# Optimization experiments

Hardware: AMD Instinct MI355X
Metric: run time of the kernel (lower is better)

The kernel has to match this reference:

```python
import jax, jax.numpy as jnp
import numpy as np
import math

N = 4264          # all_node_num
B = 256           # batch size
VIS = 784 + 50    # input_node_num + label_node_num
NG = 8            # number of color groups (Pegasus chromatic number is small)
GS = N // NG      # 533 nodes per group
SAMPLE_NUM = 10   # Gibbs sweeps (default 1000 in source; reduced for reference)
AVG_DEG = 15.0    # Pegasus graph degree ~15


def setup_inputs() -> dict:
    key = jax.random.key(0)
    k1, k2, k3, k4 = jax.random.split(key, 4)
    # spin state in {-1, +1}, shape [B, N]
    m = jnp.where(jax.random.normal(k1, (B, N)) >= 0, 1.0, -1.0).astype(jnp.float32)
    # sparse symmetric coupling matrix J: ~AVG_DEG neighbors per node, values randn*0.01
    upper_mask = jnp.triu(jax.random.uniform(k2, (N, N)) < (AVG_DEG / N), k=1)
    Jup = jax.random.normal(k3, (N, N), dtype=jnp.float32) * 0.01 * upper_mask
    J = Jup + Jup.T
    # bias H: log-odds constant on visible nodes, zero on hidden
    h_vis = math.log((VIS / N) / (1.0 - VIS / N))
    H = jnp.zeros((N,), dtype=jnp.float32).at[:VIS].set(h_vis)
    # color groups: disjoint partition of node indices, [NG, GS]
    groups = jax.random.permutation(k4, N).reshape(NG, GS).astype(jnp.int32)
    return {"m": m, "J": J, "H": H, "groups": groups, "sample_num": SAMPLE_NUM}


def reference(m, J, H, groups, sample_num):
    n_groups = groups.shape[0]

    def sweep(m, key):
        keys = jax.random.split(key, n_groups)
        for g in range(n_groups):          # small fixed set of color groups
            idx = groups[g]                # [GS]
            # I = sparse.mm(J[idx], m.T).T + H[idx]  ->  [B, GS]
            I = jnp.einsum('bn,gn->bg', m, J[idx]) + H[idx]
            r = jax.random.uniform(keys[g], I.shape, dtype=I.dtype) * 2.0 - 1.0
            m = m.at[:, idx].set(jnp.sign(jnp.tanh(I) - r))
        return m, None

    iter_keys = jax.random.split(jax.random.key(42), sample_num)
    m, _ = jax.lax.scan(sweep, m, iter_keys)
    return m
```

## Files before the change

kernel.cpp:

```cpp
#include <hip/hip_runtime.h>
#include <hip/hip_bf16.h>
#include <stdint.h>

#define NN 4264
#define BB 256
#define GSZ 533
#define NGRP 8
#define NSWEEP 10
#define NSTEP (NSWEEP * NGRP)
#define DMAX 48
#define DFIX 24
#define NF4 1066

struct Keys { unsigned k0[NSTEP]; unsigned k1[NSTEP]; };

#define TF_ROUND(x0, x1, r) { x0 += x1; x1 = (x1 << (r)) | (x1 >> (32 - (r))); x1 ^= x0; }
#define TF_BODY(K0, K1, C0, C1, O0, O1) {                                   \
  unsigned ks0 = (K0), ks1 = (K1), ks2 = (K0) ^ (K1) ^ 0x1BD11BDAu;          \
  unsigned x0 = (C0) + ks0, x1 = (C1) + ks1;                                 \
  TF_ROUND(x0, x1, 13) TF_ROUND(x0, x1, 15) TF_ROUND(x0, x1, 26) TF_ROUND(x0, x1, 6)  \
  x0 += ks1; x1 += ks2 + 1u;                                                 \
  TF_ROUND(x0, x1, 17) TF_ROUND(x0, x1, 29) TF_ROUND(x0, x1, 16) TF_ROUND(x0, x1, 24) \
  x0 += ks2; x1 += ks0 + 2u;                                                 \
  TF_ROUND(x0, x1, 13) TF_ROUND(x0, x1, 15) TF_ROUND(x0, x1, 26) TF_ROUND(x0, x1, 6)  \
  x0 += ks0; x1 += ks1 + 3u;                                                 \
  TF_ROUND(x0, x1, 17) TF_ROUND(x0, x1, 29) TF_ROUND(x0, x1, 16) TF_ROUND(x0, x1, 24) \
  x0 += ks1; x1 += ks2 + 4u;                                                 \
  TF_ROUND(x0, x1, 13) TF_ROUND(x0, x1, 15) TF_ROUND(x0, x1, 26) TF_ROUND(x0, x1, 6)  \
  x0 += ks2; x1 += ks0 + 5u;                                                 \
  (O0) = x0; (O1) = x1; }

static void tf_host(unsigned k0, unsigned k1, unsigned c0, unsigned c1,
                    unsigned* o0, unsigned* o1) {
  unsigned a, b;
  TF_BODY(k0, k1, c0, c1, a, b);
  *o0 = a; *o1 = b;
}

__device__ __forceinline__ void tf_dev(unsigned k0, unsigned k1, unsigned c0, unsigned c1,
                                       unsigned& o0, unsigned& o1) {
  TF_BODY(k0, k1, c0, c1, o0, o1);
}

__global__ __launch_bounds__(256) void build_ell(const float* __restrict__ J,
                                                 const int* __restrict__ groups,
                                                 unsigned* __restrict__ pack4,
                                                 int2* __restrict__ exact8,
                                                 int* __restrict__ deg,
                                                 float* __restrict__ marg) {
  const int wv = threadIdx.x >> 6, lane = threadIdx.x & 63;
  const int p = blockIdx.x * 4 + wv;
  if (p >= NN) return;
  const int node = groups[p];
  const float4* row = (const float4*)(J + (size_t)node * NN);
  int cnt = 0;
  float asum = 0.0f;
  for (int it = 0; it < (NF4 + 63) / 64; ++it) {
    const int q = it * 64 + lane;
    float4 v;
    if (q < NF4) v = row[q];
    else         v = make_float4(0.0f, 0.0f, 0.0f, 0.0f);
    const int c0 = q * 4;
#define COMP(X, CIDX) {                                                        \
      const bool nz = ((X) != 0.0f);                                           \
      const unsigned long long mk = __ballot(nz);                              \
      const int rk = cnt + __popcll(mk & ((1ull << lane) - 1ull));             \
      if (nz) {                                                                \
        if (rk < DFIX) {                                                       \
          const unsigned bits = __float_as_uint(X);                            \
          const unsigned bf = (bits + 0x7fffu + ((bits >> 16) & 1u)) >> 16;    \
          pack4[(size_t)p * DFIX + rk] = (bf << 16) | ((unsigned)(CIDX) << 2); \
          asum += fabsf(X);                                                    \
        }                                                                      \
        if (rk < DMAX)                                                         \
          exact8[(size_t)p * DMAX + rk] = make_int2((CIDX), __float_as_int(X));\
      }                                                                        \
      cnt += __popcll(mk); }
    COMP(v.x, c0 + 0) COMP(v.y, c0 + 1) COMP(v.z, c0 + 2) COMP(v.w, c0 + 3)
#undef COMP
  }
  for (int k = cnt + lane; k < DFIX; k += 64) pack4[(size_t)p * DFIX + k] = 0u;
  for (int s = 1; s < 64; s <<= 1) asum += __shfl_xor(asum, s, 64);
  if (lane == 0) {
    deg[p] = (cnt > DMAX) ? DMAX : cnt;
    marg[p] = asum * 0.001953125f + 2e-5f;
  }
}

__global__ __launch_bounds__(576) void gibbs(const float* __restrict__ m0,
                                             const float* __restrict__ H,
                                             const int* __restrict__ groups,
                                             const unsigned* __restrict__ pack4,
                                             const int2* __restrict__ exact8,
                                             const int* __restrict__ deg,
                                             const float* __restrict__ marg,
                                             float* __restrict__ out,
                                             Keys keys) {
  __shared__ float m_lds[NN];
  const int b = blockIdx.x;
  const int i = threadIdx.x;
  const bool active = (i < GSZ);

  for (int n = i; n < NN; n += 576) m_lds[n] = m0[(size_t)b * NN + n];

  int nodeg[NGRP];
  float hg[NGRP], mgg[NGRP];
  int dgg[NGRP];
  if (active) {
#pragma unroll
    for (int g = 0; g < NGRP; ++g) {
      const int p = g * GSZ + i;
      nodeg[g] = groups[p];
      hg[g] = H[nodeg[g]];
      dgg[g] = deg[p];
      mgg[g] = marg[p];
    }
  }
  __syncthreads();

  const unsigned c = (unsigned)(b * GSZ + i);

#pragma unroll 1
  for (int t = 0; t < NSWEEP; ++t) {
#pragma unroll
    for (int g = 0; g < NGRP; ++g) {
      const int step = t * NGRP + g;
      const unsigned k0 = keys.k0[step];
      const unsigned k1 = keys.k1[step];
      float nv = 0.0f;
      if (active) {
        const int p = g * GSZ + i;
        const uint4* q = (const uint4*)(pack4 + (size_t)p * DFIX);
        uint4 w0 = q[0], w1 = q[1], w2 = q[2], w3 = q[3], w4 = q[4], w5 = q[5];
        float a0 = 0.0f, a1 = 0.0f, a2 = 0.0f, a3 = 0.0f;
#define MV(W)  (*(const float*)((const char*)m_lds + ((W) & 0xFFFCu)))
#define ACC(W) \
        a0 += __uint_as_float((W).x & 0xFFFF0000u) * MV((W).x); \
        a1 += __uint_as_float((W).y & 0xFFFF0000u) * MV((W).y); \
        a2 += __uint_as_float((W).z & 0xFFFF0000u) * MV((W).z); \
        a3 += __uint_as_float((W).w & 0xFFFF0000u) * MV((W).w);
        ACC(w0) ACC(w1) ACC(w2) ACC(w3) ACC(w4) ACC(w5)
#undef ACC
#undef MV
        const int dg = dgg[g];
        const int2* ep = exact8 + (size_t)p * DMAX;
        if (__builtin_expect(dg > DFIX, 0)) {
          for (int k = DFIX; k < dg; ++k) {
            const int2 e = ep[k];
            a0 += __int_as_float(e.y) * m_lds[e.x];
          }
        }
        const float I = ((a0 + a1) + (a2 + a3)) + hg[g];

        unsigned o0, o1;
        tf_dev(k0, k1, 0u, c, o0, o1);
        const unsigned bits = o0 ^ o1;
        const float u = __uint_as_float((bits >> 9) | 0x3f800000u) - 1.0f;
        const float r = u * 2.0f - 1.0f;

        const float th = tanhf(I);
        const float d = th - r;
        if (__builtin_expect(fabsf(d) > mgg[g], 1)) {
          nv = (d > 0.0f) ? 1.0f : -1.0f;
        } else {
          double I64 = (double)hg[g];
          for (int k = 0; k < dg; ++k) {
            const int2 e = ep[k];
            I64 += (double)__int_as_float(e.y) * (double)m_lds[e.x];
          }
          const double diff = tanh(I64) - (double)r;
          nv = (diff > 0.0) ? 1.0f : ((diff < 0.0) ? -1.0f : 0.0f);
        }
      }
      __syncthreads();
      if (active) m_lds[nodeg[g]] = nv;
      __syncthreads();
    }
  }

  for (int n = i; n < NN; n += 576) out[(size_t)b * NN + n] = m_lds[n];
}

extern "C" void kernel_launch(void* const* d_in, const int* in_sizes, int n_in,
                              void* d_out, int out_size, void* d_ws, size_t ws_size,
                              hipStream_t stream) {
  const float* m0     = (const float*)d_in[0];
  const float* J      = (const float*)d_in[1];
  const float* H      = (const float*)d_in[2];
  const int*   groups = (const int*)d_in[3];

  char* ws = (char*)d_ws;
  unsigned* pack4  = (unsigned*)ws;                     ws += (size_t)NN * DFIX * 4;
  int2*     exact8 = (int2*)ws;                         ws += (size_t)NN * DMAX * 8;
  int*      deg    = (int*)ws;                          ws += (size_t)NN * 4;
  float*    marg   = (float*)ws;

  Keys keys;
  for (int t = 0; t < NSWEEP; ++t) {
    unsigned ik0, ik1;
    tf_host(0u, 42u, 0u, (unsigned)t, &ik0, &ik1);
    for (int g = 0; g < NGRP; ++g) {
      unsigned gk0, gk1;
      tf_host(ik0, ik1, 0u, (unsigned)g, &gk0, &gk1);
      keys.k0[t * NGRP + g] = gk0;
      keys.k1[t * NGRP + g] = gk1;
    }
  }

  build_ell<<<(NN + 3) / 4, 256, 0, stream>>>(J, groups, pack4, exact8, deg, marg);
  gibbs<<<BB, 576, 0, stream>>>(m0, H, groups, pack4, exact8, deg, marg,
                                (float*)d_out, keys);
}
```

Measured before the change: 276.2 us.

## Prefetch next group's packed couplings and hoist RNG before accumulation

In the Gibbs kernel, the packed bf16 neighbor list for the next color group is loaded into registers while the current group is being processed. The Threefry random draw is moved ahead of the LDS accumulation so its arithmetic can overlap with pending memory loads. In build_ell, all row loads are issued up front into a register array before the ballot compaction runs. The cost is higher register pressure in both kernels, which could lower occupancy or cause spills.

```diff
diff --git a/kernel.cpp b/kernel.cpp
--- a/kernel.cpp
+++ b/kernel.cpp
@@ -11,6 +11,7 @@
 #define DMAX 48
 #define DFIX 24
 #define NF4 1066
+#define NIT 17
 
 struct Keys { unsigned k0[NSTEP]; unsigned k1[NSTEP]; };
 
@@ -53,14 +54,20 @@
   if (p >= NN) return;
   const int node = groups[p];
   const float4* row = (const float4*)(J + (size_t)node * NN);
+
+  float4 vv[NIT];
+#pragma unroll
+  for (int it = 0; it < NIT; ++it) {
+    const int q = it * 64 + lane;
+    vv[it] = (q < NF4) ? row[q] : make_float4(0.0f, 0.0f, 0.0f, 0.0f);
+  }
+
   int cnt = 0;
   float asum = 0.0f;
-  for (int it = 0; it < (NF4 + 63) / 64; ++it) {
-    const int q = it * 64 + lane;
-    float4 v;
-    if (q < NF4) v = row[q];
-    else         v = make_float4(0.0f, 0.0f, 0.0f, 0.0f);
-    const int c0 = q * 4;
+#pragma unroll
+  for (int it = 0; it < NIT; ++it) {
+    const float4 v = vv[it];
+    const int c0 = (it * 64 + lane) * 4;
 #define COMP(X, CIDX) {                                                        \
       const bool nz = ((X) != 0.0f);                                           \
       const unsigned long long mk = __ballot(nz);                              \
@@ -116,9 +123,15 @@
       mgg[g] = marg[p];
     }
   }
+
+  const unsigned c = (unsigned)(b * GSZ + i);
+
+  uint4 w0, w1, w2, w3, w4, w5;
+  if (active) {
+    const uint4* q = (const uint4*)(pack4 + (size_t)(0 * GSZ + i) * DFIX);
+    w0 = q[0]; w1 = q[1]; w2 = q[2]; w3 = q[3]; w4 = q[4]; w5 = q[5];
+  }
   __syncthreads();
-
-  const unsigned c = (unsigned)(b * GSZ + i);
 
 #pragma unroll 1
   for (int t = 0; t < NSWEEP; ++t) {
@@ -128,10 +141,14 @@
       const unsigned k0 = keys.k0[step];
       const unsigned k1 = keys.k1[step];
       float nv = 0.0f;
+      uint4 n0, n1, n2, n3, n4, n5;
       if (active) {
-        const int p = g * GSZ + i;
-        const uint4* q = (const uint4*)(pack4 + (size_t)p * DFIX);
-        uint4 w0 = q[0], w1 = q[1], w2 = q[2], w3 = q[3], w4 = q[4], w5 = q[5];
+        unsigned o0, o1;
+        tf_dev(k0, k1, 0u, c, o0, o1);
+        const unsigned bits = o0 ^ o1;
+        const float u = __uint_as_float((bits >> 9) | 0x3f800000u) - 1.0f;
+        const float r = u * 2.0f - 1.0f;
+
         float a0 = 0.0f, a1 = 0.0f, a2 = 0.0f, a3 = 0.0f;
 #define MV(W)  (*(const float*)((const char*)m_lds + ((W) & 0xFFFCu)))
 #define ACC(W) \
@@ -142,8 +159,15 @@
         ACC(w0) ACC(w1) ACC(w2) ACC(w3) ACC(w4) ACC(w5)
 #undef ACC
 #undef MV
+
+        {
+          const int gn = (g + 1) & (NGRP - 1);
+          const uint4* qn = (const uint4*)(pack4 + (size_t)(gn * GSZ + i) * DFIX);
+          n0 = qn[0]; n1 = qn[1]; n2 = qn[2]; n3 = qn[3]; n4 = qn[4]; n5 = qn[5];
+        }
+
         const int dg = dgg[g];
-        const int2* ep = exact8 + (size_t)p * DMAX;
+        const int2* ep = exact8 + (size_t)(g * GSZ + i) * DMAX;
         if (__builtin_expect(dg > DFIX, 0)) {
           for (int k = DFIX; k < dg; ++k) {
             const int2 e = ep[k];
@@ -151,12 +175,6 @@
           }
         }
         const float I = ((a0 + a1) + (a2 + a3)) + hg[g];
-
-        unsigned o0, o1;
-        tf_dev(k0, k1, 0u, c, o0, o1);
-        const unsigned bits = o0 ^ o1;
-        const float u = __uint_as_float((bits >> 9) | 0x3f800000u) - 1.0f;
-        const float r = u * 2.0f - 1.0f;
 
         const float th = tanhf(I);
         const float d = th - r;
@@ -175,6 +193,7 @@
       __syncthreads();
       if (active) m_lds[nodeg[g]] = nv;
       __syncthreads();
+      w0 = n0; w1 = n1; w2 = n2; w3 = n3; w4 = n4; w5 = n5;
     }
   }
 
```

New measurement: 298.3 us. 8.0% more time.
